# Kernel tuning notes

Measured on AMD Instinct MI355X. Metric: run time of the kernel, lower is better.

Reference implementation:

```python
import jax, jax.numpy as jnp
import numpy as np

B, S = 512, 64
ZD, GD, SK = 256, 16, 512   # vel_z_dim, genre_cond_dim, skel_encode_dim
H = 1024                    # vel_hidden_dim
ND, VC = 9, 4               # n_drum_classes, vel_cond_dim


def _gru(x, h, Wi, Wh, bi, bh):
    # torch.nn.GRUCell math; gates ordered [r, z, n]
    gi = x @ Wi.T + bi
    gh = h @ Wh.T + bh
    i_r, i_z, i_n = jnp.split(gi, 3, axis=-1)
    h_r, h_z, h_n = jnp.split(gh, 3, axis=-1)
    r = jax.nn.sigmoid(i_r + h_r)
    zg = jax.nn.sigmoid(i_z + h_z)
    n = jnp.tanh(i_n + r * h_n)
    return (1.0 - zg) * n + zg * h


def setup_inputs() -> dict:
    key = jax.random.key(0)
    ks = jax.random.split(key, 14)
    rn = lambda k, shp, s: jax.random.normal(k, shp, dtype=jnp.float32) * s
    return dict(
        z=rn(ks[0], (B, ZD), 1.0),
        note_encoded=rn(ks[1], (B, SK), 1.0),
        vel_target=jax.random.uniform(ks[2], (B, S, ND), dtype=jnp.float32),
        note=jax.random.uniform(ks[3], (B, S, ND), dtype=jnp.float32),
        vel_cond=jax.random.uniform(ks[4], (B, S, VC), dtype=jnp.float32),
        genre_cond=rn(ks[5], (B, GD), 1.0),
        W_in=rn(ks[6], (H, ZD + SK + GD), 0.02), b_in=jnp.zeros((H,), jnp.float32),
        W_ih1=rn(ks[7], (3 * H, ND * 2 + VC), 0.05), W_hh1=rn(ks[8], (3 * H, H), 0.02),
        b_ih1=jnp.zeros((3 * H,), jnp.float32), b_hh1=jnp.zeros((3 * H,), jnp.float32),
        W_ih2=rn(ks[9], (3 * H, H), 0.02), W_hh2=rn(ks[10], (3 * H, H), 0.02),
        b_ih2=jnp.zeros((3 * H,), jnp.float32), b_hh2=jnp.zeros((3 * H,), jnp.float32),
        W_out=rn(ks[11], (ND, H), 0.02), b_out=jnp.zeros((ND,), jnp.float32),
        training=0, teacher_forcing_ratio=0,
    )


def reference(z, note_encoded, vel_target, note, vel_cond, genre_cond,
              W_in, b_in, W_ih1, W_hh1, b_ih1, b_hh1,
              W_ih2, W_hh2, b_ih2, b_hh2, W_out, b_out,
              training, teacher_forcing_ratio):
    # eval mode: dropout = identity, teacher forcing never taken
    del vel_target, training, teacher_forcing_ratio
    bsz = z.shape[0]
    zc = jnp.concatenate([z.reshape(bsz, -1), note_encoded, genre_cond], axis=-1)
    h1 = jnp.tanh(zc @ W_in.T + b_in)              # [B, H]
    h2 = jnp.zeros_like(h1)                        # overwritten at step 0
    out0 = jnp.zeros((bsz, W_out.shape[0]), z.dtype)

    def step(carry, xs):
        out, h1, h2 = carry
        i, nt, ct = xs
        inp = jnp.concatenate([out, nt, ct], axis=-1)       # [B, 2*ND+VC]
        h1 = _gru(inp, h1, W_ih1, W_hh1, b_ih1, b_hh1)
        h2 = jnp.where(i == 0, h1, h2)                      # hx[1] = hx[0] at i==0
        h2 = _gru(h1, h2, W_ih2, W_hh2, b_ih2, b_hh2)
        vel = jax.nn.sigmoid(h2 @ W_out.T + b_out)          # [B, ND]
        return (vel, h1, h2), vel

    xs = (jnp.arange(note.shape[1]),
          jnp.transpose(note, (1, 0, 2)),
          jnp.transpose(vel_cond, (1, 0, 2)))
    _, outs = jax.lax.scan(step, (out0, h1, h2), xs)
    return jnp.transpose(outs, (1, 0, 2))                    # [B, S, ND]
```

## Files before the change

### kernel.cpp

```cpp
#include <hip/hip_runtime.h>
#include <hip/hip_bf16.h>

#define HD 1024
#define BB 512
#define SS 64
#define N3 3072
#define NC 9216
#define ND 9
#define VC 4
#define KI 832

typedef __attribute__((ext_vector_type(8))) short bf16x8;
typedef __attribute__((ext_vector_type(4))) float f32x4;

__device__ __forceinline__ ushort f2b(float f) {
    unsigned u = __builtin_bit_cast(unsigned, f);
    u += 0x7fffu + ((u >> 16) & 1u);
    return (ushort)(u >> 16);
}

__device__ __forceinline__ float sigf(float x) {
    return 1.f / (1.f + __expf(-x));
}

__device__ __forceinline__ void gld_lds16(const void* g, void* l) {
    __builtin_amdgcn_global_load_lds(
        (const __attribute__((address_space(1))) unsigned int*)g,
        (__attribute__((address_space(3))) unsigned int*)l, 16, 0, 0);
}

__global__ __launch_bounds__(256) void prep_w(
    const float* __restrict__ Wih2, const float* __restrict__ Whh1,
    const float* __restrict__ Whh2, ushort* __restrict__ Wcat)
{
    const int row = blockIdx.x;
    const float* src = row < 3072 ? Wih2 + (size_t)row * HD
                     : row < 6144 ? Whh1 + (size_t)(row - 3072) * HD
                                  : Whh2 + (size_t)(row - 6144) * HD;
    const int c = threadIdx.x * 4;
    float4 v = *(const float4*)(src + c);
    ushort4 o;
    o.x = f2b(v.x); o.y = f2b(v.y); o.z = f2b(v.z); o.w = f2b(v.w);
    *(ushort4*)(Wcat + (size_t)row * HD + c) = o;
}

__global__ __launch_bounds__(256) void prep_wt1(
    const float* __restrict__ Wih1, float* __restrict__ Wt1)
{
    const int g = blockIdx.x * 256 + threadIdx.x;
    #pragma unroll
    for (int c = 0; c < 22; ++c)
        Wt1[c * N3 + g] = Wih1[(size_t)g * 22 + c];
}

__global__ __launch_bounds__(256) void prep_acat(
    const float* __restrict__ z, const float* __restrict__ ne,
    const float* __restrict__ gc, ushort* __restrict__ Acat)
{
    const int b = blockIdx.x;
    const int t = threadIdx.x;
    if (t >= 208) return;
    const int c = t * 4;
    float4 v = make_float4(0.f, 0.f, 0.f, 0.f);
    if (c < 256)      v = *(const float4*)(z  + (size_t)b * 256 + c);
    else if (c < 768) v = *(const float4*)(ne + (size_t)b * 512 + (c - 256));
    else if (c < 784) v = *(const float4*)(gc + (size_t)b * 16  + (c - 768));
    ushort4 o;
    o.x = f2b(v.x); o.y = f2b(v.y); o.z = f2b(v.z); o.w = f2b(v.w);
    *(ushort4*)(Acat + (size_t)b * KI + c) = o;
}

__global__ __launch_bounds__(256) void prep_win(
    const float* __restrict__ W_in, ushort* __restrict__ W_inb)
{
    const int r = blockIdx.x;
    const int t = threadIdx.x;
    if (t >= 208) return;
    const int c = t * 4;
    ushort4 o = {0, 0, 0, 0};
    if (c < 784) {
        float4 v = *(const float4*)(W_in + (size_t)r * 784 + c);
        o.x = f2b(v.x); o.y = f2b(v.y); o.z = f2b(v.z); o.w = f2b(v.w);
    }
    *(ushort4*)(W_inb + (size_t)r * KI + c) = o;
}

__global__ __launch_bounds__(256) void k_init(
    const ushort* __restrict__ Acat, const ushort* __restrict__ W_inb,
    const float* __restrict__ b_in, float* __restrict__ h1, ushort* __restrict__ h1b)
{
    __shared__ __align__(16) ushort As[2 * 4096];
    __shared__ __align__(16) ushort Bs[2 * 4096];
    const int t = blockIdx.x;
    const int nt = t >> 3, mt = t & 7;

    const int tid = threadIdx.x;
    const int w = tid >> 6, l = tid & 63;
    const int lr = l >> 3;
    const int sw = ((l & 7) ^ lr) << 3;

    const ushort* Ag0 = Acat + ((size_t)(mt << 6)) * KI + (size_t)(16 * w + lr) * KI + sw;
    const ushort* Ag1 = Ag0 + 8 * KI;
    const ushort* Bg0 = W_inb + ((size_t)(nt << 6)) * KI + (size_t)(16 * w + lr) * KI + sw;
    const ushort* Bg1 = Bg0 + 8 * KI;
    const int o0 = (16 * w) * 64, o1 = (16 * w + 8) * 64;

    gld_lds16(Ag0, As + o0); gld_lds16(Ag1, As + o1);
    gld_lds16(Bg0, Bs + o0); gld_lds16(Bg1, Bs + o1);

    const int wm = (w >> 1) << 5, wn = (w & 1) << 5;
    const int fr = l & 15, fc = l >> 4;
    const int ra0 = wm + fr, ra1 = wm + 16 + fr;
    const int rb0 = wn + fr, rb1 = wn + 16 + fr;

    f32x4 acc[2][2] = {};
    for (int kt = 0; kt < 13; ++kt) {
        const int cb = (kt & 1) << 12;
        __syncthreads();
        if (kt + 1 < 13) {
            const int nb = ((kt + 1) & 1) << 12;
            const int ko = (kt + 1) << 6;
            gld_lds16(Ag0 + ko, As + nb + o0);
            gld_lds16(Ag1 + ko, As + nb + o1);
            gld_lds16(Bg0 + ko, Bs + nb + o0);
            gld_lds16(Bg1 + ko, Bs + nb + o1);
        }
        #pragma unroll
        for (int kk = 0; kk < 2; ++kk) {
            const int c = (kk << 2) + fc;
            bf16x8 a0 = *(const bf16x8*)(As + cb + ra0 * 64 + ((c ^ (ra0 & 7)) << 3));
            bf16x8 a1 = *(const bf16x8*)(As + cb + ra1 * 64 + ((c ^ (ra1 & 7)) << 3));
            bf16x8 b0 = *(const bf16x8*)(Bs + cb + rb0 * 64 + ((c ^ (rb0 & 7)) << 3));
            bf16x8 b1 = *(const bf16x8*)(Bs + cb + rb1 * 64 + ((c ^ (rb1 & 7)) << 3));
            acc[0][0] = __builtin_amdgcn_mfma_f32_16x16x32_bf16(a0, b0, acc[0][0], 0, 0, 0);
            acc[0][1] = __builtin_amdgcn_mfma_f32_16x16x32_bf16(a0, b1, acc[0][1], 0, 0, 0);
            acc[1][0] = __builtin_amdgcn_mfma_f32_16x16x32_bf16(a1, b0, acc[1][0], 0, 0, 0);
            acc[1][1] = __builtin_amdgcn_mfma_f32_16x16x32_bf16(a1, b1, acc[1][1], 0, 0, 0);
        }
    }

    const int row0 = (mt << 6) + wm;
    const int col0 = (nt << 6) + wn + fr;
    const float b0v = b_in[col0], b1v = b_in[col0 + 16];
    #pragma unroll
    for (int i = 0; i < 2; ++i) {
        #pragma unroll
        for (int r = 0; r < 4; ++r) {
            const int row = row0 + i * 16 + fc * 4 + r;
            const float v0 = tanhf(acc[i][0][r] + b0v);
            const float v1 = tanhf(acc[i][1][r] + b1v);
            h1[(size_t)row * HD + col0]       = v0;
            h1b[(size_t)row * HD + col0]      = f2b(v0);
            h1[(size_t)row * HD + col0 + 16]  = v1;
            h1b[(size_t)row * HD + col0 + 16] = f2b(v1);
        }
    }
}

__global__ __launch_bounds__(256) void gemm3(
    const ushort* __restrict__ h1b, const ushort* __restrict__ h2b,
    const ushort* __restrict__ Wcat, float* __restrict__ Cbuf, int ntb)
{
    __shared__ __align__(16) ushort As[4096];
    __shared__ __align__(16) ushort Ws[4096];

    const int flat = blockIdx.x + (blockIdx.y << 3);
    const int id   = (flat & 7) * gridDim.y + (flat >> 3);
    const int bm   = (id & 7) << 6;
    const int nt   = (id >> 3) + ntb;

    const ushort* Amat = (nt < 96) ? h1b : h2b;
    const ushort* W    = Wcat + (size_t)(nt << 6) * HD;

    const int tid = threadIdx.x;
    const int w   = tid >> 6;
    const int l   = tid & 63;

    const int srow = l >> 3;
    const int sch  = ((l & 7) ^ srow) << 3;
    const ushort* Ag0 = Amat + (size_t)(bm + 16 * w + srow) * HD + sch;
    const ushort* Ag1 = Ag0 + 8 * HD;
    const ushort* Wg0 = W + (size_t)(16 * w + srow) * HD + sch;
    const ushort* Wg1 = Wg0 + 8 * HD;
    ushort* Al0 = As + (16 * w) * 64;
    ushort* Al1 = As + (16 * w + 8) * 64;
    ushort* Wl0 = Ws + (16 * w) * 64;
    ushort* Wl1 = Ws + (16 * w + 8) * 64;

    const int wm = (w >> 1) << 5;
    const int wn = (w & 1) << 5;
    const int fr = l & 15;
    const int fc = l >> 4;

    const int ra0 = wm + fr,  ra1 = wm + 16 + fr;
    const int rb0 = wn + fr,  rb1 = wn + 16 + fr;

    f32x4 acc00 = {0.f,0.f,0.f,0.f}, acc01 = {0.f,0.f,0.f,0.f};
    f32x4 acc10 = {0.f,0.f,0.f,0.f}, acc11 = {0.f,0.f,0.f,0.f};

    for (int kt = 0; kt < 16; ++kt) {
        const int ko = kt << 6;
        __syncthreads();
        gld_lds16(Ag0 + ko, Al0);
        gld_lds16(Ag1 + ko, Al1);
        gld_lds16(Wg0 + ko, Wl0);
        gld_lds16(Wg1 + ko, Wl1);
        __syncthreads();
        #pragma unroll
        for (int kk = 0; kk < 2; ++kk) {
            const int c = (kk << 2) + fc;
            bf16x8 a0 = *(const bf16x8*)(As + ra0 * 64 + ((c ^ (ra0 & 7)) << 3));
            bf16x8 a1 = *(const bf16x8*)(As + ra1 * 64 + ((c ^ (ra1 & 7)) << 3));
            bf16x8 b0 = *(const bf16x8*)(Ws + rb0 * 64 + ((c ^ (rb0 & 7)) << 3));
            bf16x8 b1 = *(const bf16x8*)(Ws + rb1 * 64 + ((c ^ (rb1 & 7)) << 3));
            acc00 = __builtin_amdgcn_mfma_f32_16x16x32_bf16(a0, b0, acc00, 0, 0, 0);
            acc01 = __builtin_amdgcn_mfma_f32_16x16x32_bf16(a0, b1, acc01, 0, 0, 0);
            acc10 = __builtin_amdgcn_mfma_f32_16x16x32_bf16(a1, b0, acc10, 0, 0, 0);
            acc11 = __builtin_amdgcn_mfma_f32_16x16x32_bf16(a1, b1, acc11, 0, 0, 0);
        }
    }

    const int bn = nt << 6;
    float* Cw = Cbuf + (size_t)(bm + wm) * NC + bn + wn;
    #pragma unroll
    for (int r = 0; r < 4; ++r) {
        const size_t ro0 = (size_t)(fc * 4 + r) * NC;
        const size_t ro1 = (size_t)(16 + fc * 4 + r) * NC;
        Cw[ro0 + fr]      = acc00[r];
        Cw[ro0 + 16 + fr] = acc01[r];
        Cw[ro1 + fr]      = acc10[r];
        Cw[ro1 + 16 + fr] = acc11[r];
    }
}

__global__ __launch_bounds__(1024) void gru1_first(
    const float* __restrict__ Cbuf, float* __restrict__ h1, ushort* __restrict__ h1b,
    float* __restrict__ h2, ushort* __restrict__ h2b,
    const float* __restrict__ note, const float* __restrict__ velc,
    const float* __restrict__ Wt1, const float* __restrict__ b_ih1,
    const float* __restrict__ b_hh1)
{
    __shared__ float inp[22];
    const int b = blockIdx.x;
    const int j = threadIdx.x;

    if (j < 22) {
        float v = 0.f;
        if (j >= 9 && j < 18) v = note[(size_t)b * (SS * ND) + (j - 9)];
        else if (j >= 18)     v = velc[(size_t)b * (SS * VC) + (j - 18)];
        inp[j] = v;
    }
    __syncthreads();

    float ir = b_ih1[j], iz = b_ih1[HD + j], inn = b_ih1[2 * HD + j];
    #pragma unroll
    for (int c = 0; c < 22; ++c) {
        const float x = inp[c];
        const float* wr = Wt1 + c * N3;
        ir  = fmaf(x, wr[j],          ir);
        iz  = fmaf(x, wr[HD + j],     iz);
        inn = fmaf(x, wr[2 * HD + j], inn);
    }

    const float* g = Cbuf + (size_t)b * NC + N3;
    const float hr = g[j]          + b_hh1[j];
    const float hz = g[HD + j]     + b_hh1[HD + j];
    const float hn = g[2 * HD + j] + b_hh1[2 * HD + j];

    const float rg = sigf(ir + hr);
    const float zg = sigf(iz + hz);
    const float n  = tanhf(inn + rg * hn);
    const float hnew = (1.f - zg) * n + zg * h1[(size_t)b * HD + j];
    const ushort hb = f2b(hnew);
    h1[(size_t)b * HD + j]  = hnew;
    h1b[(size_t)b * HD + j] = hb;
    h2[(size_t)b * HD + j]  = hnew;
    h2b[(size_t)b * HD + j] = hb;
}

__global__ __launch_bounds__(1024) void pw_fused(
    const float* __restrict__ Cbuf, float* __restrict__ h1, ushort* __restrict__ h1b,
    float* __restrict__ h2, ushort* __restrict__ h2b,
    const float* __restrict__ note, const float* __restrict__ velc,
    const float* __restrict__ Wt1,
    const float* __restrict__ b_ih1, const float* __restrict__ b_hh1,
    const float* __restrict__ b_ih2, const float* __restrict__ b_hh2,
    const float* __restrict__ W_out, const float* __restrict__ b_out,
    float* __restrict__ dout, int step)
{
    __shared__ float hs[2][HD];
    __shared__ float inp[2][22];
    const int j  = threadIdx.x;
    const int b0 = blockIdx.x * 2;

    if (step + 1 < SS && j < 64) {
        const int r = j >> 5, c = j & 31;
        const int b = b0 + r;
        if (c >= 9 && c < 22)
            inp[r][c] = (c < 18) ? note[(size_t)b * (SS * ND) + (step + 1) * ND + (c - 9)]
                                 : velc[(size_t)b * (SS * VC) + (step + 1) * VC + (c - 18)];
    }

    const float bir = b_ih2[j],          bhr = b_hh2[j];
    const float biz = b_ih2[HD + j],     bhz = b_hh2[HD + j];
    const float bin = b_ih2[2 * HD + j], bhn = b_hh2[2 * HD + j];

    #pragma unroll
    for (int r = 0; r < 2; ++r) {
        const int b = b0 + r;
        const float* gi = Cbuf + (size_t)b * NC;
        const float* gh = gi + 2 * N3;
        const float ir  = gi[j] + bir,          hr = gh[j] + bhr;
        const float iz  = gi[HD + j] + biz,     hz = gh[HD + j] + bhz;
        const float inn = gi[2 * HD + j] + bin, hn = gh[2 * HD + j] + bhn;
        const float rg = sigf(ir + hr);
        const float zg = sigf(iz + hz);
        const float n  = tanhf(inn + rg * hn);
        const float hnew = (1.f - zg) * n + zg * h2[(size_t)b * HD + j];
        h2[(size_t)b * HD + j]  = hnew;
        h2b[(size_t)b * HD + j] = f2b(hnew);
        hs[r][j] = hnew;
    }
    __syncthreads();

    const int w = j >> 6, t = j & 63;
    {
        const int r = w & 1, b = b0 + r;
        #pragma unroll
        for (int dd = 0; dd < 2; ++dd) {
            const int d = (w >> 1) + dd * 8;
            if (d < ND) {
                float a = 0.f;
                const float* wr = W_out + (size_t)d * HD;
                #pragma unroll
                for (int k = 0; k < HD / 64; ++k)
                    a = fmaf(hs[r][t + k * 64], wr[t + k * 64], a);
                #pragma unroll
                for (int off = 32; off > 0; off >>= 1) a += __shfl_down(a, off);
                if (t == 0) {
                    const float o = sigf(a + b_out[d]);
                    dout[(size_t)b * (SS * ND) + step * ND + d] = o;
                    inp[r][d] = o;
                }
            }
        }
    }
    __syncthreads();

    if (step + 1 < SS) {
        float xir[2], xiz[2], xinn[2];
        #pragma unroll
        for (int r = 0; r < 2; ++r) {
            xir[r] = b_ih1[j]; xiz[r] = b_ih1[HD + j]; xinn[r] = b_ih1[2 * HD + j];
        }
        #pragma unroll
        for (int c = 0; c < 22; ++c) {
            const float w0 = Wt1[c * N3 + j];
            const float w1 = Wt1[c * N3 + HD + j];
            const float w2 = Wt1[c * N3 + 2 * HD + j];
            #pragma unroll
            for (int r = 0; r < 2; ++r) {
                const float x = inp[r][c];
                xir[r]  = fmaf(x, w0, xir[r]);
                xiz[r]  = fmaf(x, w1, xiz[r]);
                xinn[r] = fmaf(x, w2, xinn[r]);
            }
        }
        #pragma unroll
        for (int r = 0; r < 2; ++r) {
            const int b = b0 + r;
            const float* g1 = Cbuf + (size_t)b * NC + N3;
            const float hr1 = g1[j]          + b_hh1[j];
            const float hz1 = g1[HD + j]     + b_hh1[HD + j];
            const float hn1 = g1[2 * HD + j] + b_hh1[2 * HD + j];
            const float rg1 = sigf(xir[r] + hr1);
            const float zg1 = sigf(xiz[r] + hz1);
            const float n1  = tanhf(xinn[r] + rg1 * hn1);
            const float h1new = (1.f - zg1) * n1 + zg1 * h1[(size_t)b * HD + j];
            h1[(size_t)b * HD + j]  = h1new;
            h1b[(size_t)b * HD + j] = f2b(h1new);
        }
    }
}

extern "C" void kernel_launch(void* const* d_in, const int* in_sizes, int n_in,
                              void* d_out, int out_size, void* d_ws, size_t ws_size,
                              hipStream_t stream)
{
    const float* z     = (const float*)d_in[0];
    const float* ne    = (const float*)d_in[1];
    const float* note  = (const float*)d_in[3];
    const float* velc  = (const float*)d_in[4];
    const float* gc    = (const float*)d_in[5];
    const float* W_in  = (const float*)d_in[6];
    const float* b_in  = (const float*)d_in[7];
    const float* W_ih1 = (const float*)d_in[8];
    const float* W_hh1 = (const float*)d_in[9];
    const float* b_ih1 = (const float*)d_in[10];
    const float* b_hh1 = (const float*)d_in[11];
    const float* W_ih2 = (const float*)d_in[12];
    const float* W_hh2 = (const float*)d_in[13];
    const float* b_ih2 = (const float*)d_in[14];
    const float* b_hh2 = (const float*)d_in[15];
    const float* W_out = (const float*)d_in[16];
    const float* b_out = (const float*)d_in[17];
    float* out = (float*)d_out;

    float*  h1   = (float*)d_ws;
    float*  h2   = h1 + BB * HD;
    float*  Cbuf = h2 + BB * HD;
    float*  Wt1  = Cbuf + (size_t)BB * NC;
    ushort* h1b  = (ushort*)(Wt1 + 22 * N3);
    ushort* h2b  = h1b + BB * HD;
    ushort* Wcat = h2b + BB * HD;
    ushort* Acat  = (ushort*)Cbuf;
    ushort* W_inb = Acat + (size_t)BB * KI;

    prep_w   <<<dim3(NC), 256, 0, stream>>>(W_ih2, W_hh1, W_hh2, Wcat);
    prep_wt1 <<<dim3(12), 256, 0, stream>>>(W_ih1, Wt1);
    prep_acat<<<dim3(BB), 256, 0, stream>>>(z, ne, gc, Acat);
    prep_win <<<dim3(HD), 256, 0, stream>>>(W_in, W_inb);

    k_init<<<dim3(128), 256, 0, stream>>>(Acat, W_inb, b_in, h1, h1b);

    gemm3<<<dim3(8, 48), 256, 0, stream>>>(h1b, h2b, Wcat, Cbuf, 48);
    gru1_first<<<dim3(BB), 1024, 0, stream>>>(Cbuf, h1, h1b, h2, h2b,
                                              note, velc, Wt1, b_ih1, b_hh1);

    for (int s = 0; s < SS; ++s) {
        gemm3<<<dim3(8, 144), 256, 0, stream>>>(h1b, h2b, Wcat, Cbuf, 0);
        pw_fused<<<dim3(BB / 2), 1024, 0, stream>>>(Cbuf, h1, h1b, h2, h2b,
                                                    note, velc, Wt1,
                                                    b_ih1, b_hh1, b_ih2, b_hh2,
                                                    W_out, b_out, out, s);
    }
}
```

Baseline: 2.000 ms.

## Triple-buffer gemm3 LDS tiles with K=32 stages and prefetch distance two

```diff
diff --git a/kernel.cpp b/kernel.cpp
--- a/kernel.cpp
+++ b/kernel.cpp
@@ -161,8 +161,8 @@
     const ushort* __restrict__ h1b, const ushort* __restrict__ h2b,
     const ushort* __restrict__ Wcat, float* __restrict__ Cbuf, int ntb)
 {
-    __shared__ __align__(16) ushort As[4096];
-    __shared__ __align__(16) ushort Ws[4096];
+    __shared__ __align__(16) ushort As[3 * 2048];
+    __shared__ __align__(16) ushort Ws[3 * 2048];
 
     const int flat = blockIdx.x + (blockIdx.y << 3);
     const int id   = (flat & 7) * gridDim.y + (flat >> 3);
@@ -176,16 +176,12 @@
     const int w   = tid >> 6;
     const int l   = tid & 63;
 
-    const int srow = l >> 3;
-    const int sch  = ((l & 7) ^ srow) << 3;
-    const ushort* Ag0 = Amat + (size_t)(bm + 16 * w + srow) * HD + sch;
-    const ushort* Ag1 = Ag0 + 8 * HD;
-    const ushort* Wg0 = W + (size_t)(16 * w + srow) * HD + sch;
-    const ushort* Wg1 = Wg0 + 8 * HD;
-    ushort* Al0 = As + (16 * w) * 64;
-    ushort* Al1 = As + (16 * w + 8) * 64;
-    ushort* Wl0 = Ws + (16 * w) * 64;
-    ushort* Wl1 = Ws + (16 * w + 8) * 64;
+    const int srow = l >> 2;
+    const int sch  = ((l & 3) ^ (srow & 3)) << 3;
+    const ushort* Ag = Amat + (size_t)(bm + 16 * w + srow) * HD + sch;
+    const ushort* Wg = W    + (size_t)(16 * w + srow) * HD + sch;
+    ushort* Al = As + (w << 9);
+    ushort* Wl = Ws + (w << 9);
 
     const int wm = (w >> 1) << 5;
     const int wn = (w & 1) << 5;
@@ -194,29 +190,42 @@
 
     const int ra0 = wm + fr,  ra1 = wm + 16 + fr;
     const int rb0 = wn + fr,  rb1 = wn + 16 + fr;
+    const int oa0 = ra0 * 32 + ((fc ^ (ra0 & 3)) << 3);
+    const int oa1 = ra1 * 32 + ((fc ^ (ra1 & 3)) << 3);
+    const int ob0 = rb0 * 32 + ((fc ^ (rb0 & 3)) << 3);
+    const int ob1 = rb1 * 32 + ((fc ^ (rb1 & 3)) << 3);
 
     f32x4 acc00 = {0.f,0.f,0.f,0.f}, acc01 = {0.f,0.f,0.f,0.f};
     f32x4 acc10 = {0.f,0.f,0.f,0.f}, acc11 = {0.f,0.f,0.f,0.f};
 
-    for (int kt = 0; kt < 16; ++kt) {
-        const int ko = kt << 6;
-        __syncthreads();
-        gld_lds16(Ag0 + ko, Al0);
-        gld_lds16(Ag1 + ko, Al1);
-        gld_lds16(Wg0 + ko, Wl0);
-        gld_lds16(Wg1 + ko, Wl1);
-        __syncthreads();
-        #pragma unroll
-        for (int kk = 0; kk < 2; ++kk) {
-            const int c = (kk << 2) + fc;
-            bf16x8 a0 = *(const bf16x8*)(As + ra0 * 64 + ((c ^ (ra0 & 7)) << 3));
-            bf16x8 a1 = *(const bf16x8*)(As + ra1 * 64 + ((c ^ (ra1 & 7)) << 3));
-            bf16x8 b0 = *(const bf16x8*)(Ws + rb0 * 64 + ((c ^ (rb0 & 7)) << 3));
-            bf16x8 b1 = *(const bf16x8*)(Ws + rb1 * 64 + ((c ^ (rb1 & 7)) << 3));
-            acc00 = __builtin_amdgcn_mfma_f32_16x16x32_bf16(a0, b0, acc00, 0, 0, 0);
-            acc01 = __builtin_amdgcn_mfma_f32_16x16x32_bf16(a0, b1, acc01, 0, 0, 0);
-            acc10 = __builtin_amdgcn_mfma_f32_16x16x32_bf16(a1, b0, acc10, 0, 0, 0);
-            acc11 = __builtin_amdgcn_mfma_f32_16x16x32_bf16(a1, b1, acc11, 0, 0, 0);
+    gld_lds16(Ag,      Al);
+    gld_lds16(Wg,      Wl);
+    gld_lds16(Ag + 32, Al + 2048);
+    gld_lds16(Wg + 32, Wl + 2048);
+
+    #pragma unroll
+    for (int kt = 0; kt < 32; ++kt) {
+        if (kt < 31) asm volatile("s_waitcnt vmcnt(2)" ::: "memory");
+        else         asm volatile("s_waitcnt vmcnt(0)" ::: "memory");
+        __builtin_amdgcn_sched_barrier(0);
+        __builtin_amdgcn_s_barrier();
+        __builtin_amdgcn_sched_barrier(0);
+
+        const int cb = (kt % 3) * 2048;
+        bf16x8 a0 = *(const bf16x8*)(As + cb + oa0);
+        bf16x8 a1 = *(const bf16x8*)(As + cb + oa1);
+        bf16x8 b0 = *(const bf16x8*)(Ws + cb + ob0);
+        bf16x8 b1 = *(const bf16x8*)(Ws + cb + ob1);
+        acc00 = __builtin_amdgcn_mfma_f32_16x16x32_bf16(a0, b0, acc00, 0, 0, 0);
+        acc01 = __builtin_amdgcn_mfma_f32_16x16x32_bf16(a0, b1, acc01, 0, 0, 0);
+        acc10 = __builtin_amdgcn_mfma_f32_16x16x32_bf16(a1, b0, acc10, 0, 0, 0);
+        acc11 = __builtin_amdgcn_mfma_f32_16x16x32_bf16(a1, b1, acc11, 0, 0, 0);
+
+        if (kt + 2 < 32) {
+            const int nb = ((kt + 2) % 3) * 2048;
+            const int ko = (kt + 2) << 5;
+            gld_lds16(Ag + ko, Al + nb);
+            gld_lds16(Wg + ko, Wl + nb);
         }
     }
 
```

After: 2.214 ms. 10.7% more time.

## Merge GRU2 r/z gate GEMMs over concatenated [h1,h2] input with K=2048

Applied to the files above, without the earlier changes.

```diff
diff --git a/kernel.cpp b/kernel.cpp
--- a/kernel.cpp
+++ b/kernel.cpp
@@ -5,10 +5,16 @@
 #define BB 512
 #define SS 64
 #define N3 3072
-#define NC 9216
+#define NC2 7168
 #define ND 9
 #define VC 4
 #define KI 832
+#define HC 2048
+
+#define WRZ_OFF  0
+#define WGIN_OFF (2048 * 2048)
+#define WGHN_OFF (WGIN_OFF + 1024 * 1024)
+#define WH1_OFF  (WGHN_OFF + 1024 * 1024)
 
 typedef __attribute__((ext_vector_type(8))) short bf16x8;
 typedef __attribute__((ext_vector_type(4))) float f32x4;
@@ -29,19 +35,40 @@
         (__attribute__((address_space(3))) unsigned int*)l, 16, 0, 0);
 }
 
-__global__ __launch_bounds__(256) void prep_w(
+__global__ __launch_bounds__(256) void prep_w2(
     const float* __restrict__ Wih2, const float* __restrict__ Whh1,
-    const float* __restrict__ Whh2, ushort* __restrict__ Wcat)
+    const float* __restrict__ Whh2, ushort* __restrict__ Wcat2)
 {
     const int row = blockIdx.x;
-    const float* src = row < 3072 ? Wih2 + (size_t)row * HD
-                     : row < 6144 ? Whh1 + (size_t)(row - 3072) * HD
-                                  : Whh2 + (size_t)(row - 6144) * HD;
     const int c = threadIdx.x * 4;
-    float4 v = *(const float4*)(src + c);
-    ushort4 o;
-    o.x = f2b(v.x); o.y = f2b(v.y); o.z = f2b(v.z); o.w = f2b(v.w);
-    *(ushort4*)(Wcat + (size_t)row * HD + c) = o;
+    if (row < 2048) {
+        float4 a = *(const float4*)(Wih2 + (size_t)row * HD + c);
+        float4 b = *(const float4*)(Whh2 + (size_t)row * HD + c);
+        ushort4 oa, ob;
+        oa.x = f2b(a.x); oa.y = f2b(a.y); oa.z = f2b(a.z); oa.w = f2b(a.w);
+        ob.x = f2b(b.x); ob.y = f2b(b.y); ob.z = f2b(b.z); ob.w = f2b(b.w);
+        ushort* dst = Wcat2 + WRZ_OFF + (size_t)row * 2048;
+        *(ushort4*)(dst + c)        = oa;
+        *(ushort4*)(dst + 1024 + c) = ob;
+    } else {
+        const float* src;
+        ushort* dst;
+        if (row < 3072) {
+            src = Wih2 + (size_t)(2048 + row - 2048) * HD + (size_t)(row - 2048) * 0;
+            src = Wih2 + (size_t)(row) * HD;
+            dst = Wcat2 + WGIN_OFF + (size_t)(row - 2048) * HD;
+        } else if (row < 4096) {
+            src = Whh2 + (size_t)(row - 3072 + 2048) * HD;
+            dst = Wcat2 + WGHN_OFF + (size_t)(row - 3072) * HD;
+        } else {
+            src = Whh1 + (size_t)(row - 4096) * HD;
+            dst = Wcat2 + WH1_OFF + (size_t)(row - 4096) * HD;
+        }
+        float4 v = *(const float4*)(src + c);
+        ushort4 o;
+        o.x = f2b(v.x); o.y = f2b(v.y); o.z = f2b(v.z); o.w = f2b(v.w);
+        *(ushort4*)(dst + c) = o;
+    }
 }
 
 __global__ __launch_bounds__(256) void prep_wt1(
@@ -87,7 +114,7 @@
 
 __global__ __launch_bounds__(256) void k_init(
     const ushort* __restrict__ Acat, const ushort* __restrict__ W_inb,
-    const float* __restrict__ b_in, float* __restrict__ h1, ushort* __restrict__ h1b)
+    const float* __restrict__ b_in, float* __restrict__ h1, ushort* __restrict__ hcat)
 {
     __shared__ __align__(16) ushort As[2 * 4096];
     __shared__ __align__(16) ushort Bs[2 * 4096];
@@ -99,9 +126,9 @@
     const int lr = l >> 3;
     const int sw = ((l & 7) ^ lr) << 3;
 
-    const ushort* Ag0 = Acat + ((size_t)(mt << 6)) * KI + (size_t)(16 * w + lr) * KI + sw;
+    const ushort* Ag0 = Acat + ((size_t)(mt << 6) + 16 * w + lr) * KI + sw;
     const ushort* Ag1 = Ag0 + 8 * KI;
-    const ushort* Bg0 = W_inb + ((size_t)(nt << 6)) * KI + (size_t)(16 * w + lr) * KI + sw;
+    const ushort* Bg0 = W_inb + ((size_t)(nt << 6) + 16 * w + lr) * KI + sw;
     const ushort* Bg1 = Bg0 + 8 * KI;
     const int o0 = (16 * w) * 64, o1 = (16 * w + 8) * 64;
 
@@ -149,28 +176,59 @@
             const int row = row0 + i * 16 + fc * 4 + r;
             const float v0 = tanhf(acc[i][0][r] + b0v);
             const float v1 = tanhf(acc[i][1][r] + b1v);
-            h1[(size_t)row * HD + col0]       = v0;
-            h1b[(size_t)row * HD + col0]      = f2b(v0);
-            h1[(size_t)row * HD + col0 + 16]  = v1;
-            h1b[(size_t)row * HD + col0 + 16] = f2b(v1);
+            h1[(size_t)row * HD + col0]        = v0;
+            hcat[(size_t)row * HC + col0]      = f2b(v0);
+            h1[(size_t)row * HD + col0 + 16]   = v1;
+            hcat[(size_t)row * HC + col0 + 16] = f2b(v1);
         }
     }
 }
 
 __global__ __launch_bounds__(256) void gemm3(
-    const ushort* __restrict__ h1b, const ushort* __restrict__ h2b,
-    const ushort* __restrict__ Wcat, float* __restrict__ Cbuf, int ntb)
+    const ushort* __restrict__ hcat, const ushort* __restrict__ Wcat2,
+    float* __restrict__ Cbuf, int ntb)
 {
     __shared__ __align__(16) ushort As[4096];
     __shared__ __align__(16) ushort Ws[4096];
 
     const int flat = blockIdx.x + (blockIdx.y << 3);
     const int id   = (flat & 7) * gridDim.y + (flat >> 3);
-    const int bm   = (id & 7) << 6;
-    const int nt   = (id >> 3) + ntb;
-
-    const ushort* Amat = (nt < 96) ? h1b : h2b;
-    const ushort* W    = Wcat + (size_t)(nt << 6) * HD;
+    const int mt   = id & 7;
+    const int ntr  = id >> 3;
+    const int bm   = mt << 6;
+
+    int kiters, wstride, koff, cbase;
+    const ushort* Wb;
+    if (ntb >= 0) {
+        kiters = 16; wstride = HD; koff = 0;
+        Wb = Wcat2 + WH1_OFF + (size_t)(ntr << 6) * HD;
+        cbase = 4096 + (ntr << 6);
+    } else {
+        const int r7 = ntr % 7, q7 = ntr / 7;
+        if (r7 == 0 || r7 == 4) {
+            const int sn = q7 * 2 + (r7 == 4 ? 1 : 0);
+            kiters = 32; wstride = 2048; koff = 0;
+            Wb = Wcat2 + WRZ_OFF + (size_t)(sn << 6) * 2048;
+            cbase = sn << 6;
+        } else {
+            const int lr = (r7 < 4) ? (r7 - 1) : (r7 - 2);
+            const int lidx = q7 * 5 + lr;
+            kiters = 16; wstride = HD;
+            if (lidx < 16) {
+                koff = 0;
+                Wb = Wcat2 + WGIN_OFF + (size_t)(lidx << 6) * HD;
+                cbase = 2048 + (lidx << 6);
+            } else if (lidx < 32) {
+                koff = 1024;
+                Wb = Wcat2 + WGHN_OFF + (size_t)((lidx - 16) << 6) * HD;
+                cbase = 3072 + ((lidx - 16) << 6);
+            } else {
+                koff = 0;
+                Wb = Wcat2 + WH1_OFF + (size_t)((lidx - 32) << 6) * HD;
+                cbase = 4096 + ((lidx - 32) << 6);
+            }
+        }
+    }
 
     const int tid = threadIdx.x;
     const int w   = tid >> 6;
@@ -178,10 +236,10 @@
 
     const int srow = l >> 3;
     const int sch  = ((l & 7) ^ srow) << 3;
-    const ushort* Ag0 = Amat + (size_t)(bm + 16 * w + srow) * HD + sch;
-    const ushort* Ag1 = Ag0 + 8 * HD;
-    const ushort* Wg0 = W + (size_t)(16 * w + srow) * HD + sch;
-    const ushort* Wg1 = Wg0 + 8 * HD;
+    const ushort* Ag0 = hcat + (size_t)(bm + 16 * w + srow) * HC + koff + sch;
+    const ushort* Ag1 = Ag0 + 8 * HC;
+    const ushort* Wg0 = Wb + (size_t)(16 * w + srow) * wstride + sch;
+    const ushort* Wg1 = Wg0 + 8 * wstride;
     ushort* Al0 = As + (16 * w) * 64;
     ushort* Al1 = As + (16 * w + 8) * 64;
     ushort* Wl0 = Ws + (16 * w) * 64;
@@ -198,7 +256,7 @@
     f32x4 acc00 = {0.f,0.f,0.f,0.f}, acc01 = {0.f,0.f,0.f,0.f};
     f32x4 acc10 = {0.f,0.f,0.f,0.f}, acc11 = {0.f,0.f,0.f,0.f};
 
-    for (int kt = 0; kt < 16; ++kt) {
+    for (int kt = 0; kt < kiters; ++kt) {
         const int ko = kt << 6;
         __syncthreads();
         gld_lds16(Ag0 + ko, Al0);
@@ -220,12 +278,11 @@
         }
     }
 
-    const int bn = nt << 6;
-    float* Cw = Cbuf + (size_t)(bm + wm) * NC + bn + wn;
+    float* Cw = Cbuf + (size_t)(bm + wm) * NC2 + cbase + wn;
     #pragma unroll
     for (int r = 0; r < 4; ++r) {
-        const size_t ro0 = (size_t)(fc * 4 + r) * NC;
-        const size_t ro1 = (size_t)(16 + fc * 4 + r) * NC;
+        const size_t ro0 = (size_t)(fc * 4 + r) * NC2;
+        const size_t ro1 = (size_t)(16 + fc * 4 + r) * NC2;
         Cw[ro0 + fr]      = acc00[r];
         Cw[ro0 + 16 + fr] = acc01[r];
         Cw[ro1 + fr]      = acc10[r];
@@ -234,8 +291,8 @@
 }
 
 __global__ __launch_bounds__(1024) void gru1_first(
-    const float* __restrict__ Cbuf, float* __restrict__ h1, ushort* __restrict__ h1b,
-    float* __restrict__ h2, ushort* __restrict__ h2b,
+    const float* __restrict__ Cbuf, float* __restrict__ h1, float* __restrict__ h2,
+    ushort* __restrict__ hcat,
     const float* __restrict__ note, const float* __restrict__ velc,
     const float* __restrict__ Wt1, const float* __restrict__ b_ih1,
     const float* __restrict__ b_hh1)
@@ -262,7 +319,7 @@
         inn = fmaf(x, wr[2 * HD + j], inn);
     }
 
-    const float* g = Cbuf + (size_t)b * NC + N3;
+    const float* g = Cbuf + (size_t)b * NC2 + 4096;
     const float hr = g[j]          + b_hh1[j];
     const float hz = g[HD + j]     + b_hh1[HD + j];
     const float hn = g[2 * HD + j] + b_hh1[2 * HD + j];
@@ -272,15 +329,15 @@
     const float n  = tanhf(inn + rg * hn);
     const float hnew = (1.f - zg) * n + zg * h1[(size_t)b * HD + j];
     const ushort hb = f2b(hnew);
-    h1[(size_t)b * HD + j]  = hnew;
-    h1b[(size_t)b * HD + j] = hb;
-    h2[(size_t)b * HD + j]  = hnew;
-    h2b[(size_t)b * HD + j] = hb;
+    h1[(size_t)b * HD + j]       = hnew;
+    h2[(size_t)b * HD + j]       = hnew;
+    hcat[(size_t)b * HC + j]     = hb;
+    hcat[(size_t)b * HC + 1024 + j] = hb;
 }
 
 __global__ __launch_bounds__(1024) void pw_fused(
-    const float* __restrict__ Cbuf, float* __restrict__ h1, ushort* __restrict__ h1b,
-    float* __restrict__ h2, ushort* __restrict__ h2b,
+    const float* __restrict__ Cbuf, float* __restrict__ h1, float* __restrict__ h2,
+    ushort* __restrict__ hcat,
     const float* __restrict__ note, const float* __restrict__ velc,
     const float* __restrict__ Wt1,
     const float* __restrict__ b_ih1, const float* __restrict__ b_hh1,
@@ -301,24 +358,25 @@
                                  : velc[(size_t)b * (SS * VC) + (step + 1) * VC + (c - 18)];
     }
 
-    const float bir = b_ih2[j],          bhr = b_hh2[j];
-    const float biz = b_ih2[HD + j],     bhz = b_hh2[HD + j];
-    const float bin = b_ih2[2 * HD + j], bhn = b_hh2[2 * HD + j];
+    const float brz = b_ih2[j]          + b_hh2[j];
+    const float bzz = b_ih2[HD + j]     + b_hh2[HD + j];
+    const float bin = b_ih2[2 * HD + j];
+    const float bhn = b_hh2[2 * HD + j];
 
     #pragma unroll
     for (int r = 0; r < 2; ++r) {
         const int b = b0 + r;
-        const float* gi = Cbuf + (size_t)b * NC;
-        const float* gh = gi + 2 * N3;
-        const float ir  = gi[j] + bir,          hr = gh[j] + bhr;
-        const float iz  = gi[HD + j] + biz,     hz = gh[HD + j] + bhz;
-        const float inn = gi[2 * HD + j] + bin, hn = gh[2 * HD + j] + bhn;
-        const float rg = sigf(ir + hr);
-        const float zg = sigf(iz + hz);
-        const float n  = tanhf(inn + rg * hn);
+        const float* cb = Cbuf + (size_t)b * NC2;
+        const float sr  = cb[j]           + brz;
+        const float sz  = cb[1024 + j]    + bzz;
+        const float gin = cb[2048 + j]    + bin;
+        const float ghn = cb[3072 + j]    + bhn;
+        const float rg = sigf(sr);
+        const float zg = sigf(sz);
+        const float n  = tanhf(gin + rg * ghn);
         const float hnew = (1.f - zg) * n + zg * h2[(size_t)b * HD + j];
-        h2[(size_t)b * HD + j]  = hnew;
-        h2b[(size_t)b * HD + j] = f2b(hnew);
+        h2[(size_t)b * HD + j] = hnew;
+        hcat[(size_t)b * HC + 1024 + j] = f2b(hnew);
         hs[r][j] = hnew;
     }
     __syncthreads();
@@ -369,7 +427,7 @@
         #pragma unroll
         for (int r = 0; r < 2; ++r) {
             const int b = b0 + r;
-            const float* g1 = Cbuf + (size_t)b * NC + N3;
+            const float* g1 = Cbuf + (size_t)b * NC2 + 4096;
             const float hr1 = g1[j]          + b_hh1[j];
             const float hz1 = g1[HD + j]     + b_hh1[HD + j];
             const float hn1 = g1[2 * HD + j] + b_hh1[2 * HD + j];
@@ -377,8 +435,8 @@
             const float zg1 = sigf(xiz[r] + hz1);
             const float n1  = tanhf(xinn[r] + rg1 * hn1);
             const float h1new = (1.f - zg1) * n1 + zg1 * h1[(size_t)b * HD + j];
-            h1[(size_t)b * HD + j]  = h1new;
-            h1b[(size_t)b * HD + j] = f2b(h1new);
+            h1[(size_t)b * HD + j] = h1new;
+            hcat[(size_t)b * HC + j] = f2b(h1new);
         }
     }
 }
@@ -406,30 +464,29 @@
     const float* b_out = (const float*)d_in[17];
     float* out = (float*)d_out;
 
-    float*  h1   = (float*)d_ws;
-    float*  h2   = h1 + BB * HD;
-    float*  Cbuf = h2 + BB * HD;
-    float*  Wt1  = Cbuf + (size_t)BB * NC;
-    ushort* h1b  = (ushort*)(Wt1 + 22 * N3);
-    ushort* h2b  = h1b + BB * HD;
-    ushort* Wcat = h2b + BB * HD;
+    float*  h1    = (float*)d_ws;
+    float*  h2    = h1 + BB * HD;
+    float*  Cbuf  = h2 + BB * HD;
+    float*  Wt1   = Cbuf + (size_t)BB * NC2;
+    ushort* hcat  = (ushort*)(Wt1 + 22 * N3);
+    ushort* Wcat2 = hcat + (size_t)BB * HC;
     ushort* Acat  = (ushort*)Cbuf;
     ushort* W_inb = Acat + (size_t)BB * KI;
 
-    prep_w   <<<dim3(NC), 256, 0, stream>>>(W_ih2, W_hh1, W_hh2, Wcat);
-    prep_wt1 <<<dim3(12), 256, 0, stream>>>(W_ih1, Wt1);
-    prep_acat<<<dim3(BB), 256, 0, stream>>>(z, ne, gc, Acat);
-    prep_win <<<dim3(HD), 256, 0, stream>>>(W_in, W_inb);
-
-    k_init<<<dim3(128), 256, 0, stream>>>(Acat, W_inb, b_in, h1, h1b);
-
-    gemm3<<<dim3(8, 48), 256, 0, stream>>>(h1b, h2b, Wcat, Cbuf, 48);
-    gru1_first<<<dim3(BB), 1024, 0, stream>>>(Cbuf, h1, h1b, h2, h2b,
+    prep_w2  <<<dim3(NC2), 256, 0, stream>>>(W_ih2, W_hh1, W_hh2, Wcat2);
+    prep_wt1 <<<dim3(12),  256, 0, stream>>>(W_ih1, Wt1);
+    prep_acat<<<dim3(BB),  256, 0, stream>>>(z, ne, gc, Acat);
+    prep_win <<<dim3(HD),  256, 0, stream>>>(W_in, W_inb);
+
+    k_init<<<dim3(128), 256, 0, stream>>>(Acat, W_inb, b_in, h1, hcat);
+
+    gemm3<<<dim3(8, 48), 256, 0, stream>>>(hcat, Wcat2, Cbuf, 0);
+    gru1_first<<<dim3(BB), 1024, 0, stream>>>(Cbuf, h1, h2, hcat,
                                               note, velc, Wt1, b_ih1, b_hh1);
 
     for (int s = 0; s < SS; ++s) {
-        gemm3<<<dim3(8, 144), 256, 0, stream>>>(h1b, h2b, Wcat, Cbuf, 0);
-        pw_fused<<<dim3(BB / 2), 1024, 0, stream>>>(Cbuf, h1, h1b, h2, h2b,
+        gemm3<<<dim3(8, 112), 256, 0, stream>>>(hcat, Wcat2, Cbuf, -1);
+        pw_fused<<<dim3(BB / 2), 1024, 0, stream>>>(Cbuf, h1, h2, hcat,
                                                     note, velc, Wt1,
                                                     b_ih1, b_hh1, b_ih2, b_hh2,
                                                     W_out, b_out, out, s);
```

Measured after the change: 2.391 ms. 19.5% more time.
